# Optimization experiments

Hardware: AMD Instinct MI355X
Metric: run time of the kernel (lower is better)

The kernel has to match this reference:

```python
import jax, jax.numpy as jnp
import numpy as np

N, M, P = 8192, 8192, 16


def setup_inputs() -> dict:
    key = jax.random.key(0)
    k1, k2, k3, k4, k5 = jax.random.split(key, 5)
    x1 = jax.random.normal(k1, (N, P), dtype=jnp.float32)
    x2 = jax.random.normal(k2, (M, P), dtype=jnp.float32)
    # flax initializers.uniform() draws in [0, 0.01); use small scalars
    log_sigma_b = jax.random.uniform(k3, (), dtype=jnp.float32) * 0.01
    log_sigma_v = jax.random.uniform(k4, (), dtype=jnp.float32) * 0.01
    offset = jax.random.uniform(k5, (), dtype=jnp.float32) * 0.01
    return {"x1": x1, "x2": x2, "log_sigma_b": log_sigma_b,
            "log_sigma_v": log_sigma_v, "offset": offset}


def reference(x1, x2, log_sigma_b, log_sigma_v, offset):
    sigma_b = jnp.exp(log_sigma_b)
    sigma_v = jnp.exp(log_sigma_v)
    # sum_p (x1-offset)(x2-offset) as a dot product (n,p)@(p,m) -> (n,m)
    d = jnp.einsum("np,mp->nm", x1 - offset, x2 - offset)
    K = sigma_v ** 2 * d + sigma_b ** 2
    return K
```

## Files before the change

### kernel.cpp

```cpp
#include <hip/hip_runtime.h>
#include <cmath>


#define TILE 128
#define LDST 132

__global__ __launch_bounds__(256) void linear_kernel(
    const float* __restrict__ x1, const float* __restrict__ x2,
    const float* __restrict__ p_lsb, const float* __restrict__ p_lsv,
    const float* __restrict__ p_off, float* __restrict__ out, int ldout)
{
    __shared__ float s1[16 * LDST];
    __shared__ float s2[16 * LDST];

    const int tid = threadIdx.x;
    const int tx = tid & 15;
    const int ty = tid >> 4;
    const int n0 = blockIdx.y * TILE;
    const int m0 = blockIdx.x * TILE;

    const float off = p_off[0];
    const float sb  = expf(p_lsb[0]);
    const float sv  = expf(p_lsv[0]);
    const float sv2 = sv * sv;
    const float sb2 = sb * sb;

    const float4* g1 = (const float4*)(x1 + (size_t)n0 * 16);
    const float4* g2 = (const float4*)(x2 + (size_t)m0 * 16);
    #pragma unroll
    for (int j = tid; j < 512; j += 256) {
        const int row = j >> 2;
        const int p0  = (j & 3) * 4;
        float4 v = g1[j];
        s1[(p0 + 0) * LDST + row] = v.x - off;
        s1[(p0 + 1) * LDST + row] = v.y - off;
        s1[(p0 + 2) * LDST + row] = v.z - off;
        s1[(p0 + 3) * LDST + row] = v.w - off;
        float4 w = g2[j];
        s2[(p0 + 0) * LDST + row] = w.x - off;
        s2[(p0 + 1) * LDST + row] = w.y - off;
        s2[(p0 + 2) * LDST + row] = w.z - off;
        s2[(p0 + 3) * LDST + row] = w.w - off;
    }

    float acc[8][8];
    #pragma unroll
    for (int r = 0; r < 8; ++r)
        #pragma unroll
        for (int c = 0; c < 8; ++c) acc[r][c] = 0.0f;

    __syncthreads();

    #pragma unroll
    for (int p = 0; p < 16; ++p) {
        const float* s1p = &s1[p * LDST];
        const float* s2p = &s2[p * LDST];
        const float4 a0 = *(const float4*)&s1p[ty * 4];
        const float4 a1 = *(const float4*)&s1p[64 + ty * 4];
        const float4 b0 = *(const float4*)&s2p[tx * 4];
        const float4 b1 = *(const float4*)&s2p[64 + tx * 4];
        const float av[8] = {a0.x, a0.y, a0.z, a0.w, a1.x, a1.y, a1.z, a1.w};
        const float bv[8] = {b0.x, b0.y, b0.z, b0.w, b1.x, b1.y, b1.z, b1.w};
        #pragma unroll
        for (int r = 0; r < 8; ++r)
            #pragma unroll
            for (int c = 0; c < 8; ++c)
                acc[r][c] += av[r] * bv[c];
    }

    #pragma unroll
    for (int r = 0; r < 8; ++r) {
        const int lr  = (r < 4) ? (ty * 4 + r) : (64 + ty * 4 + (r - 4));
        float* orow = out + (size_t)(n0 + lr) * (size_t)ldout + m0;
        float4 o0, o1;
        o0.x = sv2 * acc[r][0] + sb2;
        o0.y = sv2 * acc[r][1] + sb2;
        o0.z = sv2 * acc[r][2] + sb2;
        o0.w = sv2 * acc[r][3] + sb2;
        o1.x = sv2 * acc[r][4] + sb2;
        o1.y = sv2 * acc[r][5] + sb2;
        o1.z = sv2 * acc[r][6] + sb2;
        o1.w = sv2 * acc[r][7] + sb2;
        *(float4*)&orow[tx * 4]      = o0;
        *(float4*)&orow[64 + tx * 4] = o1;
    }
}

extern "C" void kernel_launch(void* const* d_in, const int* in_sizes, int n_in,
                              void* d_out, int out_size, void* d_ws, size_t ws_size,
                              hipStream_t stream) {
    const float* x1  = (const float*)d_in[0];
    const float* x2  = (const float*)d_in[1];
    const float* lsb = (const float*)d_in[2];
    const float* lsv = (const float*)d_in[3];
    const float* off = (const float*)d_in[4];
    float* out = (float*)d_out;

    const int n = in_sizes[0] / 16;
    const int m = in_sizes[1] / 16;

    dim3 grid(m / TILE, n / TILE);
    linear_kernel<<<grid, 256, 0, stream>>>(x1, x2, lsb, lsv, off, out, m);
}
```

Baseline: 273.5 us.

## Split into transpose prep kernel and LDS-direct-load GEMM with nontemporal stores

Adds a prep kernel that subtracts the offset, scales by sigma_v and writes transposed (P-major) copies of x1 and x2 to workspace. The GEMM kernel then fills LDS with direct global-to-LDS loads, uses a 128x256 tile with 512 threads where each wave owns 16 rows and each lane 4 columns, and writes output with nontemporal stores. The aim is to cut staging overhead and cache pollution on the write-bound 256MB output. The cost is an extra kernel launch and a pass over the inputs, plus the per-thread A values become wave-broadcast LDS reads.

```diff
diff --git a/kernel.cpp b/kernel.cpp
--- a/kernel.cpp
+++ b/kernel.cpp
@@ -2,87 +2,109 @@
 #include <cmath>
 
 
-#define TILE 128
-#define LDST 132
+typedef float f32x4 __attribute__((ext_vector_type(4)));
 
-__global__ __launch_bounds__(256) void linear_kernel(
+__device__ __forceinline__ void gload_lds16(const float* g, float* l) {
+    __builtin_amdgcn_global_load_lds(
+        (const __attribute__((address_space(1))) void*)g,
+        (__attribute__((address_space(3))) void*)l, 16, 0, 0);
+}
+
+__global__ __launch_bounds__(256) void prep_kernel(
     const float* __restrict__ x1, const float* __restrict__ x2,
-    const float* __restrict__ p_lsb, const float* __restrict__ p_lsv,
-    const float* __restrict__ p_off, float* __restrict__ out, int ldout)
+    const float* __restrict__ p_lsv, const float* __restrict__ p_off,
+    float* __restrict__ a_t, float* __restrict__ b_t, int n, int m)
 {
-    __shared__ float s1[16 * LDST];
-    __shared__ float s2[16 * LDST];
+    const float off = p_off[0];
+    const float sv  = expf(p_lsv[0]);
 
-    const int tid = threadIdx.x;
-    const int tx = tid & 15;
-    const int ty = tid >> 4;
-    const int n0 = blockIdx.y * TILE;
-    const int m0 = blockIdx.x * TILE;
+    int b = blockIdx.x;
+    const int nb = n >> 8;
+    const float* src; float* dst; int rows;
+    if (b < nb) { src = x1; dst = a_t; rows = n; }
+    else        { b -= nb; src = x2; dst = b_t; rows = m; }
 
-    const float off = p_off[0];
+    const int r = (b << 8) + threadIdx.x;
+    const f32x4* g = (const f32x4*)(src + (size_t)r * 16);
+    float vals[16];
+    #pragma unroll
+    for (int q = 0; q < 4; ++q) {
+        f32x4 v = g[q];
+        #pragma unroll
+        for (int j = 0; j < 4; ++j) vals[q * 4 + j] = v[j];
+    }
+    #pragma unroll
+    for (int p = 0; p < 16; ++p)
+        dst[(size_t)p * rows + r] = sv * (vals[p] - off);
+}
+
+__global__ __launch_bounds__(512, 4) void gemm_kernel(
+    const float* __restrict__ a_t, const float* __restrict__ b_t,
+    const float* __restrict__ p_lsb, float* __restrict__ out, int n, int m)
+{
+    __shared__ float s1[16 * 128];
+    __shared__ float s2[16 * 256];
+
+    const int tid  = threadIdx.x;
+    const int lane = tid & 63;
+    const int wid  = tid >> 6;
+    const int n0 = blockIdx.y * 128;
+    const int m0 = blockIdx.x * 256;
+
+    {
+        const float* g0 = b_t + (size_t)wid * m + m0 + (lane << 2);
+        gload_lds16(g0, &s2[wid * 256]);
+        const float* g1 = b_t + (size_t)(wid + 8) * m + m0 + (lane << 2);
+        gload_lds16(g1, &s2[(wid + 8) * 256]);
+        const int pr = (wid << 1) + (lane >> 5);
+        const float* g2 = a_t + (size_t)pr * n + n0 + ((lane & 31) << 2);
+        gload_lds16(g2, &s1[(wid << 1) * 128]);
+    }
+
     const float sb  = expf(p_lsb[0]);
-    const float sv  = expf(p_lsv[0]);
-    const float sv2 = sv * sv;
     const float sb2 = sb * sb;
 
-    const float4* g1 = (const float4*)(x1 + (size_t)n0 * 16);
-    const float4* g2 = (const float4*)(x2 + (size_t)m0 * 16);
+    float acc[16][4];
     #pragma unroll
-    for (int j = tid; j < 512; j += 256) {
-        const int row = j >> 2;
-        const int p0  = (j & 3) * 4;
-        float4 v = g1[j];
-        s1[(p0 + 0) * LDST + row] = v.x - off;
-        s1[(p0 + 1) * LDST + row] = v.y - off;
-        s1[(p0 + 2) * LDST + row] = v.z - off;
-        s1[(p0 + 3) * LDST + row] = v.w - off;
-        float4 w = g2[j];
-        s2[(p0 + 0) * LDST + row] = w.x - off;
-        s2[(p0 + 1) * LDST + row] = w.y - off;
-        s2[(p0 + 2) * LDST + row] = w.z - off;
-        s2[(p0 + 3) * LDST + row] = w.w - off;
-    }
-
-    float acc[8][8];
-    #pragma unroll
-    for (int r = 0; r < 8; ++r)
+    for (int r = 0; r < 16; ++r)
         #pragma unroll
-        for (int c = 0; c < 8; ++c) acc[r][c] = 0.0f;
+        for (int c = 0; c < 4; ++c) acc[r][c] = 0.0f;
 
     __syncthreads();
 
     #pragma unroll
     for (int p = 0; p < 16; ++p) {
-        const float* s1p = &s1[p * LDST];
-        const float* s2p = &s2[p * LDST];
-        const float4 a0 = *(const float4*)&s1p[ty * 4];
-        const float4 a1 = *(const float4*)&s1p[64 + ty * 4];
-        const float4 b0 = *(const float4*)&s2p[tx * 4];
-        const float4 b1 = *(const float4*)&s2p[64 + tx * 4];
-        const float av[8] = {a0.x, a0.y, a0.z, a0.w, a1.x, a1.y, a1.z, a1.w};
-        const float bv[8] = {b0.x, b0.y, b0.z, b0.w, b1.x, b1.y, b1.z, b1.w};
+        const f32x4 b4 = *(const f32x4*)&s2[p * 256 + (lane << 2)];
+        const float* ap = &s1[p * 128 + (wid << 4)];
+        const f32x4 a0 = *(const f32x4*)(ap + 0);
+        const f32x4 a1 = *(const f32x4*)(ap + 4);
+        const f32x4 a2 = *(const f32x4*)(ap + 8);
+        const f32x4 a3 = *(const f32x4*)(ap + 12);
+        float av[16];
         #pragma unroll
-        for (int r = 0; r < 8; ++r)
+        for (int j = 0; j < 4; ++j) {
+            av[j]      = a0[j];
+            av[4 + j]  = a1[j];
+            av[8 + j]  = a2[j];
+            av[12 + j] = a3[j];
+        }
+        #pragma unroll
+        for (int r = 0; r < 16; ++r)
             #pragma unroll
-            for (int c = 0; c < 8; ++c)
-                acc[r][c] += av[r] * bv[c];
+            for (int c = 0; c < 4; ++c)
+                acc[r][c] += av[r] * b4[c];
     }
 
+    float* op = out + (size_t)(n0 + (wid << 4)) * m + m0 + (lane << 2);
     #pragma unroll
-    for (int r = 0; r < 8; ++r) {
-        const int lr  = (r < 4) ? (ty * 4 + r) : (64 + ty * 4 + (r - 4));
-        float* orow = out + (size_t)(n0 + lr) * (size_t)ldout + m0;
-        float4 o0, o1;
-        o0.x = sv2 * acc[r][0] + sb2;
-        o0.y = sv2 * acc[r][1] + sb2;
-        o0.z = sv2 * acc[r][2] + sb2;
-        o0.w = sv2 * acc[r][3] + sb2;
-        o1.x = sv2 * acc[r][4] + sb2;
-        o1.y = sv2 * acc[r][5] + sb2;
-        o1.z = sv2 * acc[r][6] + sb2;
-        o1.w = sv2 * acc[r][7] + sb2;
-        *(float4*)&orow[tx * 4]      = o0;
-        *(float4*)&orow[64 + tx * 4] = o1;
+    for (int r = 0; r < 16; ++r) {
+        f32x4 o;
+        o[0] = acc[r][0] + sb2;
+        o[1] = acc[r][1] + sb2;
+        o[2] = acc[r][2] + sb2;
+        o[3] = acc[r][3] + sb2;
+        __builtin_nontemporal_store(o, (f32x4*)op);
+        op += m;
     }
 }
 
@@ -99,6 +121,11 @@
     const int n = in_sizes[0] / 16;
     const int m = in_sizes[1] / 16;
 
-    dim3 grid(m / TILE, n / TILE);
-    linear_kernel<<<grid, 256, 0, stream>>>(x1, x2, lsb, lsv, off, out, m);
+    float* a_t = (float*)d_ws;
+    float* b_t = a_t + (size_t)16 * n;
+
+    prep_kernel<<<dim3((n + m) / 256), 256, 0, stream>>>(x1, x2, lsv, off,
+                                                         a_t, b_t, n, m);
+    gemm_kernel<<<dim3(m / 256, n / 128), 512, 0, stream>>>(a_t, b_t, lsb,
+                                                            out, n, m);
 }
```

Measured after the change: 284.9 us. 1.04x slower.
